# Optimization experiments

Hardware: AMD Instinct MI355X
Metric: run time of the kernel (lower is better)

## Reference

```python
import jax, jax.numpy as jnp
import numpy as np

HEADS = 8
HEAD_DIM = 64
SCALE = (2 * HEAD_DIM) ** -0.5


def setup_inputs() -> dict:
    key = jax.random.key(0)
    k1, k2, k3, k4, k5 = jax.random.split(key, 5)
    B, N, D = 2, 2048, 512
    inner = HEADS * HEAD_DIM  # 512
    return {
        "x1": jax.random.normal(k1, (B, N, D), dtype=jnp.float32),
        "x2": jax.random.normal(k2, (B, N, D), dtype=jnp.float32),
        "W_qkv1": jax.random.normal(k3, (D, 3 * inner), dtype=jnp.float32) * 0.02,
        "W_qkv2": jax.random.normal(k4, (D, 3 * inner), dtype=jnp.float32) * 0.02,
        "W_out": jax.random.normal(k5, (inner, D), dtype=jnp.float32) * 0.02,
        "b_out": jnp.zeros((D,), dtype=jnp.float32),
    }


def _split_heads(t):
    # [b, n, h*d] -> [b, h, n, d]
    b, n, hd = t.shape
    return t.reshape(b, n, HEADS, HEAD_DIM).transpose(0, 2, 1, 3)


def reference(x1, x2, W_qkv1, W_qkv2, W_out, b_out):
    qkv1 = x1 @ W_qkv1  # [b, n, 3*inner]
    qkv2 = x2 @ W_qkv2
    q1, k1, v1 = (_split_heads(t) for t in jnp.split(qkv1, 3, axis=-1))
    q2, k2, v2 = (_split_heads(t) for t in jnp.split(qkv2, 3, axis=-1))

    # fused dual-stream logits: scale * (q1 k1^T + q2 k2^T)  [b, h, n, n]
    dots = SCALE * (jnp.einsum("bhnd,bhmd->bhnm", q1, k1)
                    + jnp.einsum("bhnd,bhmd->bhnm", q2, k2))
    attn = jax.nn.softmax(dots, axis=-1)

    out1 = jnp.einsum("bhnm,bhmd->bhnd", attn, v1)
    out2 = jnp.einsum("bhnm,bhmd->bhnd", attn, v2)

    def _merge(t):
        b, h, n, d = t.shape
        return t.transpose(0, 2, 1, 3).reshape(b, n, h * d)

    out = jnp.concatenate([_merge(out1), _merge(out2)], axis=1)  # [b, 2n, inner]
    return out @ W_out + b_out
```

## Files before the change

### kernel.cpp

```cpp
#include <hip/hip_runtime.h>
#include <hip/hip_bf16.h>

typedef __attribute__((ext_vector_type(8))) short bf16x8;
typedef __attribute__((ext_vector_type(4))) float f32x4;
typedef __attribute__((ext_vector_type(16))) float f32x16;
typedef __attribute__((ext_vector_type(4))) short s16x4;
typedef __attribute__((ext_vector_type(4))) int i32x4;

#define MFMA(a, b, c) __builtin_amdgcn_mfma_f32_16x16x32_bf16(a, b, c, 0, 0, 0)
#define MFMA32(a, b, c) __builtin_amdgcn_mfma_f32_32x32x16_bf16(a, b, c, 0, 0, 0)

#define SCALE_F 0.08838834764831845f

__device__ __forceinline__ short f2bf(float f) {
  __hip_bfloat16 h = __float2bfloat16(f);
  return *reinterpret_cast<short*>(&h);
}

__device__ __forceinline__ void gld_lds16(const void* g, void* s) {
  __builtin_amdgcn_global_load_lds(
      (const __attribute__((address_space(1))) void*)g,
      (__attribute__((address_space(3))) void*)s, 16, 0, 0);
}

__global__ void cast_bf16_dual(const float* __restrict__ a,
                               const float* __restrict__ b,
                               short* __restrict__ oa, short* __restrict__ ob,
                               int n) {
  int idx = (blockIdx.x * 256 + threadIdx.x) * 4;
  const float* src = a;
  short* dst = oa;
  if (idx >= n) { idx -= n; src = b; dst = ob; }
  float4 v = *(const float4*)&src[idx];
  s16x4 o;
  o.x = f2bf(v.x); o.y = f2bf(v.y); o.z = f2bf(v.z); o.w = f2bf(v.w);
  *(s16x4*)&dst[idx] = o;
}

__global__ void cast_transpose3(const float* __restrict__ Wq1,
                                const float* __restrict__ Wq2,
                                const float* __restrict__ Wo,
                                short* __restrict__ W1t,
                                short* __restrict__ W2t,
                                short* __restrict__ Wot) {
  int i = blockIdx.x * 256 + threadIdx.x;
  const float* src;
  short* dst;
  int C;
  if (i < 786432) {
    src = Wq1; dst = W1t; C = 1536;
  } else if (i < 1572864) {
    i -= 786432; src = Wq2; dst = W2t; C = 1536;
  } else {
    i -= 1572864;
    if (i >= 262144) return;
    src = Wo; dst = Wot; C = 512;
  }
  int r = i / C, c = i % C;
  float v = src[i];
  if (C == 1536 && c < 512) v *= SCALE_F;
  dst[(size_t)c * 512 + r] = f2bf(v);
}

__global__ __launch_bounds__(256) void gemm_qkv(
    const short* __restrict__ xb1, const short* __restrict__ xb2,
    const short* __restrict__ W1t, const short* __restrict__ W2t,
    short* __restrict__ QK1, short* __restrict__ QK2,
    short* __restrict__ Vt1, short* __restrict__ Vt2) {
  __shared__ short As[128 * 64];
  __shared__ short Bs[128 * 64];
  const int tid = threadIdx.x;
  const int w = tid >> 6, l = tid & 63;
  const int sid = blockIdx.y >= 12;
  const short* A = sid ? xb2 : xb1;
  const short* Bt = sid ? W2t : W1t;
  short* C0 = sid ? QK2 : QK1;
  short* C1 = sid ? Vt2 : Vt1;
  const int m0 = blockIdx.x * 128;
  const int n0 = (sid ? blockIdx.y - 12 : blockIdx.y) * 128;
  const int mi = (w >> 1) * 64, ni = (w & 1) * 64;
  const int lrow = l & 15, lk8 = (l >> 4) * 8;
  const int K = 512;

  f32x4 acc[4][4] = {};

  for (int k0 = 0; k0 < K; k0 += 64) {
    for (int g = 0; g < 4; ++g) {
      int c = g * 256 + w * 64 + l;
      int row = c >> 3, c8 = (c & 7) * 8;
      int ldsoff = (g * 256 + w * 64) * 8;
      gld_lds16(A + (size_t)(m0 + row) * K + k0 + c8, (void*)(As + ldsoff));
      gld_lds16(Bt + (size_t)(n0 + row) * K + k0 + c8, (void*)(Bs + ldsoff));
    }
    __syncthreads();
    __builtin_amdgcn_s_setprio(1);
    for (int kp = 0; kp < 2; ++kp) {
      bf16x8 af[4], bfr[4];
      for (int mf = 0; mf < 4; ++mf)
        af[mf] = *(const bf16x8*)&As[(mi + mf * 16 + lrow) * 64 + kp * 32 + lk8];
      for (int nf = 0; nf < 4; ++nf)
        bfr[nf] = *(const bf16x8*)&Bs[(ni + nf * 16 + lrow) * 64 + kp * 32 + lk8];
      for (int mf = 0; mf < 4; ++mf)
        for (int nf = 0; nf < 4; ++nf)
          acc[mf][nf] = MFMA(af[mf], bfr[nf], acc[mf][nf]);
    }
    __builtin_amdgcn_s_setprio(0);
    __syncthreads();
  }

  for (int mf = 0; mf < 4; ++mf)
    for (int nf = 0; nf < 4; ++nf)
      for (int r = 0; r < 4; ++r) {
        int row = m0 + mi + mf * 16 + (l >> 4) * 4 + r;
        int col = n0 + ni + nf * 16 + lrow;
        float v = acc[mf][nf][r];
        if (col < 1024) {
          C0[(size_t)row * 1024 + col] = f2bf(v);
        } else {
          int b = row >> 11, n = row & 2047;
          int cv = col - 1024, h = cv >> 6, d = cv & 63;
          C1[(((size_t)(b * 8 + h) * 64 + d) << 11) + n] = f2bf(v);
        }
      }
}

__global__ __launch_bounds__(256) void gemm_out(const short* __restrict__ A,
                                                const short* __restrict__ Bt,
                                                float* __restrict__ Cf,
                                                const float* __restrict__ bias) {
  __shared__ short As[64 * 64];
  __shared__ short Bs[128 * 64];
  const int tid = threadIdx.x;
  const int w = tid >> 6, l = tid & 63;
  const int m0 = blockIdx.x * 64, n0 = blockIdx.y * 128;
  const int mi = (w >> 1) * 32, ni = (w & 1) * 64;
  const int lrow = l & 15, lk8 = (l >> 4) * 8;
  const int K = 512, N = 512;

  f32x4 acc[2][4] = {};

  for (int k0 = 0; k0 < K; k0 += 64) {
    for (int g = 0; g < 2; ++g) {
      int c = g * 256 + tid;
      int row = c >> 3, c8 = (c & 7) * 8;
      gld_lds16(A + (size_t)(m0 + row) * K + k0 + c8, (void*)(As + c * 8));
    }
    for (int g = 0; g < 4; ++g) {
      int c = g * 256 + tid;
      int row = c >> 3, c8 = (c & 7) * 8;
      gld_lds16(Bt + (size_t)(n0 + row) * K + k0 + c8, (void*)(Bs + c * 8));
    }
    __syncthreads();
    __builtin_amdgcn_s_setprio(1);
    for (int kp = 0; kp < 2; ++kp) {
      bf16x8 af[2], bfr[4];
      for (int mf = 0; mf < 2; ++mf)
        af[mf] = *(const bf16x8*)&As[(mi + mf * 16 + lrow) * 64 + kp * 32 + lk8];
      for (int nf = 0; nf < 4; ++nf)
        bfr[nf] = *(const bf16x8*)&Bs[(ni + nf * 16 + lrow) * 64 + kp * 32 + lk8];
      for (int mf = 0; mf < 2; ++mf)
        for (int nf = 0; nf < 4; ++nf)
          acc[mf][nf] = MFMA(af[mf], bfr[nf], acc[mf][nf]);
    }
    __builtin_amdgcn_s_setprio(0);
    __syncthreads();
  }

  for (int mf = 0; mf < 2; ++mf)
    for (int nf = 0; nf < 4; ++nf)
      for (int r = 0; r < 4; ++r) {
        int row = m0 + mi + mf * 16 + (l >> 4) * 4 + r;
        int col = n0 + ni + nf * 16 + lrow;
        Cf[(size_t)row * N + col] = acc[mf][nf][r] + bias[col];
      }
}

__global__ __launch_bounds__(256, 2) void attn_kernel(
    const short* __restrict__ QK1, const short* __restrict__ QK2,
    const short* __restrict__ Vt1, const short* __restrict__ Vt2,
    short* __restrict__ Ocat) {
  __shared__ short lds[32768];
  short* K1s = lds;
  short* K2s = lds + 8192;
  short* V1s = lds + 16384;
  short* V2s = lds + 24576;

  const int tid = threadIdx.x;
  const int w = tid >> 6, l = tid & 63;
  const int wq = w & 1, wk = w >> 1;
  const int lq = l & 31, hi = l >> 5;
  const int qb = blockIdx.x, bh = blockIdx.y;
  const int b = bh >> 3, h = bh & 7;

  const short* Q1p = QK1 + (size_t)b * 2048 * 1024 + h * 64;
  const short* K1p = Q1p + 512;
  const short* Q2p = QK2 + (size_t)b * 2048 * 1024 + h * 64;
  const short* K2p = Q2p + 512;
  const short* V1p = Vt1 + (size_t)bh * 64 * 2048;
  const short* V2p = Vt2 + (size_t)bh * 64 * 2048;

  const int qrow = qb * 64 + wq * 32 + lq;
  bf16x8 q1f[4], q2f[4];
#pragma unroll
  for (int ck = 0; ck < 4; ++ck) {
    q1f[ck] = *(const bf16x8*)&Q1p[(size_t)qrow * 1024 + ck * 16 + hi * 8];
    q2f[ck] = *(const bf16x8*)&Q2p[(size_t)qrow * 1024 + ck * 16 + hi * 8];
  }

  f32x16 o1a = {}, o1b = {}, o2a = {}, o2b = {};
  float mrun = -1e30f, lrun = 0.f;

  auto stage = [&](int buf, int kt) {
    const int kv0 = kt * 64;
#pragma unroll
    for (int gg = 0; gg < 2; ++gg) {
      int cl = gg * 256 + tid;
      int row = cl >> 3;
      int lc = (cl & 7) ^ (row & 7);
      int lr = row & 31;
      int krow = kv0 + ((row >> 5) << 5) + (((lr >> 3) & 1) << 4) +
                 (((lr >> 2) & 1) << 3) + (((lr >> 4) & 1) << 2) + (lr & 3);
      int doff = buf * 4096 + cl * 8;
      gld_lds16(K1p + (size_t)krow * 1024 + lc * 8, (void*)(K1s + doff));
      gld_lds16(K2p + (size_t)krow * 1024 + lc * 8, (void*)(K2s + doff));
      gld_lds16(V1p + (size_t)row * 2048 + kv0 + lc * 8, (void*)(V1s + doff));
      gld_lds16(V2p + (size_t)row * 2048 + kv0 + lc * 8, (void*)(V2s + doff));
    }
  };
  auto swo = [&](int row, int kc) { return row * 64 + ((kc ^ (row & 7)) * 8); };

  int cur = 0;
  stage(0, 0);

  for (int kt = 0; kt < 32; ++kt) {
    if (kt + 1 < 32) {
      stage(cur ^ 1, kt + 1);
      asm volatile("s_waitcnt vmcnt(8)" ::: "memory");
    } else {
      asm volatile("s_waitcnt vmcnt(0)" ::: "memory");
    }
    __builtin_amdgcn_s_barrier();

    const int krd = 32 * wk + lq;
    f32x16 s = {};
    __builtin_amdgcn_s_setprio(1);
#pragma unroll
    for (int ck = 0; ck < 4; ++ck) {
      bf16x8 k1 = *(const bf16x8*)&K1s[cur * 4096 + swo(krd, 2 * ck + hi)];
      bf16x8 k2 = *(const bf16x8*)&K2s[cur * 4096 + swo(krd, 2 * ck + hi)];
      s = MFMA32(k1, q1f[ck], s);
      s = MFMA32(k2, q2f[ck], s);
    }
    __builtin_amdgcn_s_setprio(0);

    float mx = s[0];
#pragma unroll
    for (int i = 1; i < 16; ++i) mx = fmaxf(mx, s[i]);
    if (!__all(mx - mrun <= 8.0f)) {
      float rm = fmaxf(mx, __shfl_xor(mx, 32));
      float newm = fmaxf(mrun, rm);
      float corr = __expf(mrun - newm);
      mrun = newm;
      lrun *= corr;
#pragma unroll
      for (int i = 0; i < 16; ++i) {
        o1a[i] *= corr; o1b[i] *= corr; o2a[i] *= corr; o2b[i] *= corr;
      }
    }
    float p[16];
#pragma unroll
    for (int i = 0; i < 16; ++i) { p[i] = __expf(s[i] - mrun); lrun += p[i]; }

    __hip_bfloat162 a0 = __float22bfloat162_rn(float2{p[0], p[1]});
    __hip_bfloat162 a1 = __float22bfloat162_rn(float2{p[2], p[3]});
    __hip_bfloat162 a2 = __float22bfloat162_rn(float2{p[8], p[9]});
    __hip_bfloat162 a3 = __float22bfloat162_rn(float2{p[10], p[11]});
    __hip_bfloat162 b0 = __float22bfloat162_rn(float2{p[4], p[5]});
    __hip_bfloat162 b1 = __float22bfloat162_rn(float2{p[6], p[7]});
    __hip_bfloat162 b2 = __float22bfloat162_rn(float2{p[12], p[13]});
    __hip_bfloat162 b3 = __float22bfloat162_rn(float2{p[14], p[15]});
    i32x4 w0 = {*(int*)&a0, *(int*)&a1, *(int*)&a2, *(int*)&a3};
    i32x4 w1 = {*(int*)&b0, *(int*)&b1, *(int*)&b2, *(int*)&b3};
    bf16x8 pb0 = *(bf16x8*)&w0, pb1 = *(bf16x8*)&w1;

    __builtin_amdgcn_s_setprio(1);
#pragma unroll
    for (int c = 0; c < 2; ++c) {
      bf16x8 pb = c ? pb1 : pb0;
      int kcv = 4 * wk + 2 * c + hi;
      bf16x8 v1a = *(const bf16x8*)&V1s[cur * 4096 + swo(lq, kcv)];
      bf16x8 v1b = *(const bf16x8*)&V1s[cur * 4096 + swo(32 + lq, kcv)];
      bf16x8 v2a = *(const bf16x8*)&V2s[cur * 4096 + swo(lq, kcv)];
      bf16x8 v2b = *(const bf16x8*)&V2s[cur * 4096 + swo(32 + lq, kcv)];
      o1a = MFMA32(v1a, pb, o1a);
      o1b = MFMA32(v1b, pb, o1b);
      o2a = MFMA32(v2a, pb, o2a);
      o2b = MFMA32(v2b, pb, o2b);
    }
    __builtin_amdgcn_s_setprio(0);

    asm volatile("s_waitcnt lgkmcnt(0)" ::: "memory");
    __builtin_amdgcn_s_barrier();
    cur ^= 1;
  }

  lrun += __shfl_xor(lrun, 32);
  float* cb = (float*)lds;
  float* rg = cb + wq * 4224;
  if (wk == 1) {
#pragma unroll
    for (int i = 0; i < 16; ++i) {
      rg[i * 64 + l] = o1a[i];
      rg[(16 + i) * 64 + l] = o1b[i];
      rg[(32 + i) * 64 + l] = o2a[i];
      rg[(48 + i) * 64 + l] = o2b[i];
    }
    rg[4096 + l] = mrun;
    rg[4160 + l] = lrun;
  }
  __syncthreads();
  if (wk == 0) {
    float m1 = rg[4096 + l], l1 = rg[4160 + l];
    float mstar = fmaxf(mrun, m1);
    float e0 = __expf(mrun - mstar), e1 = __expf(m1 - mstar);
    float inv = 1.0f / (lrun * e0 + l1 * e1);
    float av0 = e0 * inv, av1 = e1 * inv;
#pragma unroll
    for (int i = 0; i < 16; ++i) {
      o1a[i] = o1a[i] * av0 + rg[i * 64 + l] * av1;
      o1b[i] = o1b[i] * av0 + rg[(16 + i) * 64 + l] * av1;
      o2a[i] = o2a[i] * av0 + rg[(32 + i) * 64 + l] * av1;
      o2b[i] = o2b[i] * av0 + rg[(48 + i) * 64 + l] * av1;
    }
    const size_t base1 = ((size_t)b * 4096 + qrow) * 512 + h * 64;
    const size_t base2 = base1 + (size_t)2048 * 512;
#pragma unroll
    for (int rq = 0; rq < 4; ++rq) {
      int d0 = 8 * rq + 4 * hi;
      s16x4 ov;
      ov.x = f2bf(o1a[rq * 4 + 0]); ov.y = f2bf(o1a[rq * 4 + 1]);
      ov.z = f2bf(o1a[rq * 4 + 2]); ov.w = f2bf(o1a[rq * 4 + 3]);
      *(s16x4*)&Ocat[base1 + d0] = ov;
      ov.x = f2bf(o1b[rq * 4 + 0]); ov.y = f2bf(o1b[rq * 4 + 1]);
      ov.z = f2bf(o1b[rq * 4 + 2]); ov.w = f2bf(o1b[rq * 4 + 3]);
      *(s16x4*)&Ocat[base1 + 32 + d0] = ov;
      ov.x = f2bf(o2a[rq * 4 + 0]); ov.y = f2bf(o2a[rq * 4 + 1]);
      ov.z = f2bf(o2a[rq * 4 + 2]); ov.w = f2bf(o2a[rq * 4 + 3]);
      *(s16x4*)&Ocat[base2 + d0] = ov;
      ov.x = f2bf(o2b[rq * 4 + 0]); ov.y = f2bf(o2b[rq * 4 + 1]);
      ov.z = f2bf(o2b[rq * 4 + 2]); ov.w = f2bf(o2b[rq * 4 + 3]);
      *(s16x4*)&Ocat[base2 + 32 + d0] = ov;
    }
  }
}

extern "C" void kernel_launch(void* const* d_in, const int* in_sizes, int n_in,
                              void* d_out, int out_size, void* d_ws,
                              size_t ws_size, hipStream_t stream) {
  const float* x1 = (const float*)d_in[0];
  const float* x2 = (const float*)d_in[1];
  const float* Wq1 = (const float*)d_in[2];
  const float* Wq2 = (const float*)d_in[3];
  const float* Wo = (const float*)d_in[4];
  const float* bo = (const float*)d_in[5];
  float* out = (float*)d_out;

  short* p = (short*)d_ws;
  short* xb1 = p;  p += (size_t)4096 * 512;
  short* xb2 = p;  p += (size_t)4096 * 512;
  short* W1t = p;  p += (size_t)1536 * 512;
  short* W2t = p;  p += (size_t)1536 * 512;
  short* Wot = p;  p += (size_t)512 * 512;
  short* QK1 = p;  p += (size_t)4096 * 1024;
  short* QK2 = p;  p += (size_t)4096 * 1024;
  short* Vt1 = p;  p += (size_t)2 * 8 * 64 * 2048;
  short* Vt2 = p;  p += (size_t)2 * 8 * 64 * 2048;
  short* Ocat = p; p += (size_t)8192 * 512;

  cast_bf16_dual<<<4096, 256, 0, stream>>>(x1, x2, xb1, xb2, 4096 * 512);
  cast_transpose3<<<7168, 256, 0, stream>>>(Wq1, Wq2, Wo, W1t, W2t, Wot);

  gemm_qkv<<<dim3(32, 24), 256, 0, stream>>>(xb1, xb2, W1t, W2t, QK1, QK2,
                                             Vt1, Vt2);

  attn_kernel<<<dim3(32, 16), 256, 0, stream>>>(QK1, QK2, Vt1, Vt2, Ocat);

  gemm_out<<<dim3(128, 4), 256, 0, stream>>>(Ocat, Wot, out, bo);
}
```

Before: 109.8 us.

## Software-pipeline QK and softmax-PV across KV tiles; tile the weight transpose

The attention loop now splits K and V staging and computes the QK^T tile for step t+1 while running softmax and PV for step t, with K and V loads issued at separate barriers. The goal is to overlap MFMA work with the softmax VALU work and with global-to-LDS loads. Separately, the weight cast-transpose now goes through a padded LDS tile so both reads and writes are coalesced, replacing strided scalar stores. The pipelined loop carries an extra score accumulator in registers and relies on hand-written vmcnt counts that must match the number of outstanding loads.

```diff
diff --git a/kernel.cpp b/kernel.cpp
--- a/kernel.cpp
+++ b/kernel.cpp
@@ -37,29 +37,51 @@
   *(s16x4*)&dst[idx] = o;
 }
 
-__global__ void cast_transpose3(const float* __restrict__ Wq1,
-                                const float* __restrict__ Wq2,
-                                const float* __restrict__ Wo,
-                                short* __restrict__ W1t,
-                                short* __restrict__ W2t,
-                                short* __restrict__ Wot) {
-  int i = blockIdx.x * 256 + threadIdx.x;
+__global__ __launch_bounds__(256) void cast_transpose_tiled(
+    const float* __restrict__ Wq1, const float* __restrict__ Wq2,
+    const float* __restrict__ Wo, short* __restrict__ W1t,
+    short* __restrict__ W2t, short* __restrict__ Wot) {
+  __shared__ float t[64][65];
+  int bid = blockIdx.x;
   const float* src;
   short* dst;
-  int C;
-  if (i < 786432) {
-    src = Wq1; dst = W1t; C = 1536;
-  } else if (i < 1572864) {
-    i -= 786432; src = Wq2; dst = W2t; C = 1536;
+  int C, r0, c0;
+  bool isq;
+  if (bid < 384) {
+    src = (bid < 192) ? Wq1 : Wq2;
+    dst = (bid < 192) ? W1t : W2t;
+    int tb = bid % 192;
+    C = 1536; isq = true;
+    r0 = (tb / 24) * 64; c0 = (tb % 24) * 64;
   } else {
-    i -= 1572864;
-    if (i >= 262144) return;
-    src = Wo; dst = Wot; C = 512;
-  }
-  int r = i / C, c = i % C;
-  float v = src[i];
-  if (C == 1536 && c < 512) v *= SCALE_F;
-  dst[(size_t)c * 512 + r] = f2bf(v);
+    src = Wo; dst = Wot;
+    int tb = bid - 384;
+    C = 512; isq = false;
+    r0 = (tb / 8) * 64; c0 = (tb % 8) * 64;
+  }
+  const int tid = threadIdx.x;
+  const int lr = tid >> 4, lc = (tid & 15) * 4;
+#pragma unroll
+  for (int i = 0; i < 4; ++i) {
+    float4 v = *(const float4*)&src[(size_t)(r0 + lr + 16 * i) * C + c0 + lc];
+    t[lr + 16 * i][lc + 0] = v.x;
+    t[lr + 16 * i][lc + 1] = v.y;
+    t[lr + 16 * i][lc + 2] = v.z;
+    t[lr + 16 * i][lc + 3] = v.w;
+  }
+  __syncthreads();
+  const int oc = tid >> 2, orr = (tid & 3) * 16;
+  const float sc = (isq && (c0 + oc) < 512) ? SCALE_F : 1.0f;
+  short* dbase = dst + (size_t)(c0 + oc) * 512 + r0 + orr;
+#pragma unroll
+  for (int jj = 0; jj < 4; ++jj) {
+    s16x4 ov;
+    ov.x = f2bf(t[orr + 4 * jj + 0][oc] * sc);
+    ov.y = f2bf(t[orr + 4 * jj + 1][oc] * sc);
+    ov.z = f2bf(t[orr + 4 * jj + 2][oc] * sc);
+    ov.w = f2bf(t[orr + 4 * jj + 3][oc] * sc);
+    *(s16x4*)&dbase[4 * jj] = ov;
+  }
 }
 
 __global__ __launch_bounds__(256) void gemm_qkv(
@@ -210,7 +232,7 @@
   f32x16 o1a = {}, o1b = {}, o2a = {}, o2b = {};
   float mrun = -1e30f, lrun = 0.f;
 
-  auto stage = [&](int buf, int kt) {
+  auto stage_K = [&](int buf, int kt) {
     const int kv0 = kt * 64;
 #pragma unroll
     for (int gg = 0; gg < 2; ++gg) {
@@ -223,36 +245,38 @@
       int doff = buf * 4096 + cl * 8;
       gld_lds16(K1p + (size_t)krow * 1024 + lc * 8, (void*)(K1s + doff));
       gld_lds16(K2p + (size_t)krow * 1024 + lc * 8, (void*)(K2s + doff));
+    }
+  };
+  auto stage_V = [&](int buf, int kt) {
+    const int kv0 = kt * 64;
+#pragma unroll
+    for (int gg = 0; gg < 2; ++gg) {
+      int cl = gg * 256 + tid;
+      int row = cl >> 3;
+      int lc = (cl & 7) ^ (row & 7);
+      int doff = buf * 4096 + cl * 8;
       gld_lds16(V1p + (size_t)row * 2048 + kv0 + lc * 8, (void*)(V1s + doff));
       gld_lds16(V2p + (size_t)row * 2048 + kv0 + lc * 8, (void*)(V2s + doff));
     }
   };
   auto swo = [&](int row, int kc) { return row * 64 + ((kc ^ (row & 7)) * 8); };
 
-  int cur = 0;
-  stage(0, 0);
-
-  for (int kt = 0; kt < 32; ++kt) {
-    if (kt + 1 < 32) {
-      stage(cur ^ 1, kt + 1);
-      asm volatile("s_waitcnt vmcnt(8)" ::: "memory");
-    } else {
-      asm volatile("s_waitcnt vmcnt(0)" ::: "memory");
-    }
-    __builtin_amdgcn_s_barrier();
-
+  auto qk_tile = [&](int buf) -> f32x16 {
     const int krd = 32 * wk + lq;
     f32x16 s = {};
     __builtin_amdgcn_s_setprio(1);
 #pragma unroll
     for (int ck = 0; ck < 4; ++ck) {
-      bf16x8 k1 = *(const bf16x8*)&K1s[cur * 4096 + swo(krd, 2 * ck + hi)];
-      bf16x8 k2 = *(const bf16x8*)&K2s[cur * 4096 + swo(krd, 2 * ck + hi)];
+      bf16x8 k1 = *(const bf16x8*)&K1s[buf * 4096 + swo(krd, 2 * ck + hi)];
+      bf16x8 k2 = *(const bf16x8*)&K2s[buf * 4096 + swo(krd, 2 * ck + hi)];
       s = MFMA32(k1, q1f[ck], s);
       s = MFMA32(k2, q2f[ck], s);
     }
     __builtin_amdgcn_s_setprio(0);
-
+    return s;
+  };
+
+  auto smpv = [&](int buf, f32x16 s) {
     float mx = s[0];
 #pragma unroll
     for (int i = 1; i < 16; ++i) mx = fmaxf(mx, s[i]);
@@ -288,21 +312,42 @@
     for (int c = 0; c < 2; ++c) {
       bf16x8 pb = c ? pb1 : pb0;
       int kcv = 4 * wk + 2 * c + hi;
-      bf16x8 v1a = *(const bf16x8*)&V1s[cur * 4096 + swo(lq, kcv)];
-      bf16x8 v1b = *(const bf16x8*)&V1s[cur * 4096 + swo(32 + lq, kcv)];
-      bf16x8 v2a = *(const bf16x8*)&V2s[cur * 4096 + swo(lq, kcv)];
-      bf16x8 v2b = *(const bf16x8*)&V2s[cur * 4096 + swo(32 + lq, kcv)];
+      bf16x8 v1a = *(const bf16x8*)&V1s[buf * 4096 + swo(lq, kcv)];
+      bf16x8 v1b = *(const bf16x8*)&V1s[buf * 4096 + swo(32 + lq, kcv)];
+      bf16x8 v2a = *(const bf16x8*)&V2s[buf * 4096 + swo(lq, kcv)];
+      bf16x8 v2b = *(const bf16x8*)&V2s[buf * 4096 + swo(32 + lq, kcv)];
       o1a = MFMA32(v1a, pb, o1a);
       o1b = MFMA32(v1b, pb, o1b);
       o2a = MFMA32(v2a, pb, o2a);
       o2b = MFMA32(v2b, pb, o2b);
     }
     __builtin_amdgcn_s_setprio(0);
-
+  };
+
+  stage_K(0, 0);
+  stage_V(0, 0);
+  stage_K(1, 1);
+  asm volatile("s_waitcnt vmcnt(4)" ::: "memory");
+  __builtin_amdgcn_s_barrier();
+  f32x16 sprev = qk_tile(0);
+  stage_V(1, 1);
+
+  int cur = 0;
+  for (int t = 0; t < 31; ++t) {
+    asm volatile("s_waitcnt vmcnt(4) lgkmcnt(0)" ::: "memory");
+    __builtin_amdgcn_s_barrier();
+    if (t < 30) stage_K(cur, t + 2);
+    f32x16 snew = qk_tile(cur ^ 1);
+    smpv(cur, sprev);
     asm volatile("s_waitcnt lgkmcnt(0)" ::: "memory");
     __builtin_amdgcn_s_barrier();
+    if (t < 30) stage_V(cur, t + 2);
+    sprev = snew;
     cur ^= 1;
   }
+  asm volatile("s_waitcnt vmcnt(0)" ::: "memory");
+  __builtin_amdgcn_s_barrier();
+  smpv(cur, sprev);
 
   lrun += __shfl_xor(lrun, 32);
   float* cb = (float*)lds;
@@ -378,7 +423,7 @@
   short* Ocat = p; p += (size_t)8192 * 512;
 
   cast_bf16_dual<<<4096, 256, 0, stream>>>(x1, x2, xb1, xb2, 4096 * 512);
-  cast_transpose3<<<7168, 256, 0, stream>>>(Wq1, Wq2, Wo, W1t, W2t, Wot);
+  cast_transpose_tiled<<<448, 256, 0, stream>>>(Wq1, Wq2, Wo, W1t, W2t, Wot);
 
   gemm_qkv<<<dim3(32, 24), 256, 0, stream>>>(xb1, xb2, W1t, W2t, QK1, QK2,
                                              Vt1, Vt2);
```

New measurement: 102.3 us. 6.8% less time.
